# Optimization experiments

Measured on AMD Instinct MI355X. Metric: run time of the kernel, lower is better.

The kernel has to match this reference:

```python
import jax, jax.numpy as jnp
import numpy as np

B = 131072
UNITS = 256
INPUT_DIM = 256


def setup_inputs() -> dict:
    key = jax.random.key(0)
    ks = jax.random.split(key, 8)
    x = jax.random.normal(ks[0], (B, INPUT_DIM), dtype=jnp.float32)
    h_prev = jax.random.normal(ks[1], (B, UNITS), dtype=jnp.float32)
    c_prev = jax.random.normal(ks[2], (B, UNITS), dtype=jnp.float32)
    # glorot-like scale for W: fan_in = INPUT_DIM + UNITS, fan_out = 4*UNITS
    scale = jnp.sqrt(2.0 / (INPUT_DIM + UNITS + 4 * UNITS)).astype(jnp.float32)
    W = jax.random.normal(ks[3], (INPUT_DIM + UNITS, 4 * UNITS), dtype=jnp.float32) * scale
    # bias: zeros except forget gate initialized to 1.0
    b = jnp.concatenate([
        jnp.zeros(UNITS, jnp.float32),
        jnp.ones(UNITS, jnp.float32),
        jnp.zeros(UNITS, jnp.float32),
        jnp.zeros(UNITS, jnp.float32),
    ])
    peephole_i = jax.random.normal(ks[4], (UNITS,), dtype=jnp.float32) * 0.05
    peephole_f = jax.random.normal(ks[5], (UNITS,), dtype=jnp.float32) * 0.05
    peephole_o = jax.random.normal(ks[6], (UNITS,), dtype=jnp.float32) * 0.05
    return {
        "x": x, "h_prev": h_prev, "c_prev": c_prev,
        "W": W, "b": b,
        "peephole_i": peephole_i, "peephole_f": peephole_f, "peephole_o": peephole_o,
    }


def reference(x, h_prev, c_prev, W, b, peephole_i, peephole_f, peephole_o):
    combined = jnp.concatenate([x, h_prev], axis=-1)          # [B, INPUT_DIM+UNITS]
    z = combined @ W + b                                      # [B, 4*UNITS]
    i, f, c_hat, o = jnp.split(z, 4, axis=1)                  # each [B, UNITS]
    i = jax.nn.sigmoid(i + peephole_i * c_prev)
    f = jax.nn.sigmoid(f + peephole_f * c_prev)
    o = jax.nn.sigmoid(o + peephole_o * c_prev)
    c_hat = jnp.tanh(c_hat)
    c = f * c_prev + i * c_hat
    h = o * jnp.tanh(c)
    return (h, h, c)  # matches (output, [h, c]) of the Keras cell
```

## Files before the change

kernel.cpp:

```cpp
#include <hip/hip_runtime.h>
#include <cstdint>

#define NROWS   131072
#define NUNITS  256
#define KTOT    512
#define BM      128
#define THREADS 512

typedef float f32x4  __attribute__((ext_vector_type(4)));
typedef short bf16x8 __attribute__((ext_vector_type(8)));

__device__ __forceinline__ short f2bf(float x) {
    unsigned u = __float_as_uint(x);
    u += 0x7FFFu + ((u >> 16) & 1u);
    return (short)(u >> 16);
}

__global__ void convert_W_kernel(const float* __restrict__ W, short* __restrict__ Wws) {
    int i = blockIdx.x * 256 + threadIdx.x;
    int k = i >> 10;
    int c = i & 1023;
    Wws[((size_t)(k >> 5) << 15) + ((size_t)c << 5) + (k & 31)] = f2bf(W[i]);
}

__global__ void __launch_bounds__(THREADS, 4)
lstm_main_kernel(const float* __restrict__ x, const float* __restrict__ h_prev,
                 const float* __restrict__ c_prev, const float* __restrict__ bias,
                 const float* __restrict__ pi, const float* __restrict__ pf,
                 const float* __restrict__ po, const short* __restrict__ Wws,
                 float* __restrict__ out) {
    __shared__ short Ab[2][4096];
    __shared__ short Bb[3][8192];

    const int bid = blockIdx.x;
    const int swz = (bid & 7) * 512 + (bid >> 3);
    const int ut  = swz & 3;
    const int rt  = swz >> 2;
    const int row0 = rt * BM;

    const int t    = threadIdx.x;
    const int lane = t & 63;
    const int w    = t >> 6;
    const int lr   = lane & 15;
    const int hi   = lane >> 4;
    const int rh   = w >> 2;
    const int q    = w & 3;

    const int arow = t >> 2, ag = t & 3;
    const int avoff = ((row0 + arow) * 256 + ag * 8) * 4;
    const int awr   = arow * 32 + ((ag ^ ((arow >> 1) & 3)) * 8);

    const int u0  = (t >> 2) & 63;
    const int bg0 = t >> 8;
    const int bsw = ((t & 3) ^ ((t >> 3) & 3)) * 8;
    const int bvoff0 = (((bg0    ) * 256 + ut * 64 + u0) * 32 + bsw) * 2;
    const int bvoff1 = (((bg0 + 2) * 256 + ut * 64 + u0) * 32 + bsw) * 2;

    const int sw   = (hi ^ ((lr >> 1) & 3)) * 8;
    const int aoff = (rh * 64 + lr) * 32 + sw;
    const int boff = (q * 16 + lr) * 32 + sw;

    f32x4 acc[4][4];
    #pragma unroll
    for (int m = 0; m < 4; ++m)
        #pragma unroll
        for (int g = 0; g < 4; ++g)
            acc[m][g] = (f32x4){0.f, 0.f, 0.f, 0.f};

    f32x4 sreg[2];
    auto glbA = [&](int p) {
        const char* base = (const char*)(p < 8 ? x : h_prev) + ((p & 7) << 7);
        sreg[0] = *(const f32x4*)(base + avoff);
        sreg[1] = *(const f32x4*)(base + avoff + 16);
    };
    auto writeA = [&](int buf) {
        unsigned u0_, u1_, u2_, u3_;
        asm("v_cvt_pk_bf16_f32 %0, %1, %2" : "=v"(u0_) : "v"(sreg[0][0]), "v"(sreg[0][1]));
        asm("v_cvt_pk_bf16_f32 %0, %1, %2" : "=v"(u1_) : "v"(sreg[0][2]), "v"(sreg[0][3]));
        asm("v_cvt_pk_bf16_f32 %0, %1, %2" : "=v"(u2_) : "v"(sreg[1][0]), "v"(sreg[1][1]));
        asm("v_cvt_pk_bf16_f32 %0, %1, %2" : "=v"(u3_) : "v"(sreg[1][2]), "v"(sreg[1][3]));
        int4 v = make_int4((int)u0_, (int)u1_, (int)u2_, (int)u3_);
        *(int4*)&Ab[buf][awr] = v;
    };
    auto dmaB = [&](int p, int buf) {
        const char* wb = (const char*)Wws + ((size_t)p << 16);
        short* dst = &Bb[buf][0];
        __builtin_amdgcn_global_load_lds(
            (const __attribute__((address_space(1))) uint32_t*)(const void*)(wb + bvoff0),
            (__attribute__((address_space(3))) uint32_t*)(void*)(dst + t * 8), 16, 0, 0);
        __builtin_amdgcn_global_load_lds(
            (const __attribute__((address_space(1))) uint32_t*)(const void*)(wb + bvoff1),
            (__attribute__((address_space(3))) uint32_t*)(void*)(dst + 4096 + t * 8), 16, 0, 0);
    };
    auto compute = [&](int bufA, int bufB) {
        const short* A = &Ab[bufA][0];
        const short* B = &Bb[bufB][0];
        bf16x8 af[4], bfr[4];
        #pragma unroll
        for (int m = 0; m < 4; ++m)
            af[m] = *(const bf16x8*)&A[aoff + m * 512];
        #pragma unroll
        for (int g = 0; g < 4; ++g)
            bfr[g] = *(const bf16x8*)&B[boff + g * 2048];
        __builtin_amdgcn_s_setprio(1);
        #pragma unroll
        for (int g = 0; g < 4; ++g)
            #pragma unroll
            for (int m = 0; m < 4; ++m)
                acc[m][g] = __builtin_amdgcn_mfma_f32_16x16x32_bf16(af[m], bfr[g], acc[m][g], 0, 0, 0);
        __builtin_amdgcn_s_setprio(0);
    };

    glbA(0);
    dmaB(0, 0);
    dmaB(1, 1);
    writeA(0);
    asm volatile("s_waitcnt vmcnt(2) lgkmcnt(0)" ::: "memory");
    __builtin_amdgcn_s_barrier();

    #pragma unroll 2
    for (int p = 0; p < 16; ++p) {
        const int ca = p & 1, na = ca ^ 1;
        if (p < 15) glbA(p + 1);
        if (p < 14) dmaB(p + 2, (p + 2) % 3);
        compute(ca, p % 3);
        if (p < 15) {
            writeA(na);
            if (p < 14) { asm volatile("s_waitcnt vmcnt(2) lgkmcnt(0)" ::: "memory"); }
            else        { asm volatile("s_waitcnt vmcnt(0) lgkmcnt(0)" ::: "memory"); }
            __builtin_amdgcn_s_barrier();
        }
    }

    const size_t HS = (size_t)NROWS * NUNITS;
    const int u = ut * 64 + q * 16 + lr;
    const float bi = bias[u],       bfg = bias[256 + u];
    const float bc = bias[512 + u], bo  = bias[768 + u];
    const float ppi = pi[u], ppf = pf[u], ppo = po[u];
    #pragma unroll
    for (int m = 0; m < 4; ++m) {
        #pragma unroll
        for (int r = 0; r < 4; ++r) {
            const int row = row0 + rh * 64 + m * 16 + hi * 4 + r;
            const size_t o = (size_t)row * NUNITS + u;
            const float cp = c_prev[o];
            float zi = acc[m][0][r] + bi  + ppi * cp;
            float zf = acc[m][1][r] + bfg + ppf * cp;
            float zc = acc[m][2][r] + bc;
            float zo = acc[m][3][r] + bo  + ppo * cp;
            float ig = 1.f / (1.f + __expf(-zi));
            float fg = 1.f / (1.f + __expf(-zf));
            float og = 1.f / (1.f + __expf(-zo));
            zc = fminf(fmaxf(zc, -30.f), 30.f);
            float e2 = __expf(2.f * zc);
            float chat = (e2 - 1.f) / (e2 + 1.f);
            float c  = fg * cp + ig * chat;
            float ccl = fminf(fmaxf(c, -30.f), 30.f);
            float e3 = __expf(2.f * ccl);
            float th = (e3 - 1.f) / (e3 + 1.f);
            float h  = og * th;
            out[o]          = h;
            out[HS + o]     = h;
            out[2 * HS + o] = c;
        }
    }
}

extern "C" void kernel_launch(void* const* d_in, const int* in_sizes, int n_in,
                              void* d_out, int out_size, void* d_ws, size_t ws_size,
                              hipStream_t stream) {
    const float* x  = (const float*)d_in[0];
    const float* h  = (const float*)d_in[1];
    const float* c  = (const float*)d_in[2];
    const float* W  = (const float*)d_in[3];
    const float* b  = (const float*)d_in[4];
    const float* pi = (const float*)d_in[5];
    const float* pf = (const float*)d_in[6];
    const float* po = (const float*)d_in[7];
    float* out = (float*)d_out;

    short* Wws = (short*)d_ws;

    hipLaunchKernelGGL(convert_W_kernel, dim3(2048), dim3(256), 0, stream, W, Wws);
    hipLaunchKernelGGL(lstm_main_kernel, dim3(NROWS / BM * 4), dim3(THREADS), 0, stream,
                       x, h, c, b, pi, pf, po, Wws, out);
}
```

Measured before the change: 307.7 us.

## Double-buffer W tiles and prefetch activation registers two stages ahead

Replaces the triple-buffered LDS ring for W tiles with a double buffer. Activation global loads are now issued two k-steps ahead into a pair of register slots, and the next stage's A and B tiles are written before the current compute instead of after it. Dropping the third B buffer cuts shared memory per block, which may let more blocks share a CU. The trade-off is a shorter B prefetch distance and higher register pressure from the extra staging registers and the fully unrolled loop.

Result: faster. 301.7 us (median of 3 runs) (-2.0%).

```diff
diff --git a/kernel.cpp b/kernel.cpp
--- a/kernel.cpp
+++ b/kernel.cpp
@@ -30,7 +30,7 @@
                  const float* __restrict__ po, const short* __restrict__ Wws,
                  float* __restrict__ out) {
     __shared__ short Ab[2][4096];
-    __shared__ short Bb[3][8192];
+    __shared__ short Bb[2][8192];
 
     const int bid = blockIdx.x;
     const int swz = (bid & 7) * 512 + (bid >> 3);
@@ -67,24 +67,25 @@
         for (int g = 0; g < 4; ++g)
             acc[m][g] = (f32x4){0.f, 0.f, 0.f, 0.f};
 
-    f32x4 sreg[2];
+    f32x4 sreg[2][2];
     auto glbA = [&](int p) {
         const char* base = (const char*)(p < 8 ? x : h_prev) + ((p & 7) << 7);
-        sreg[0] = *(const f32x4*)(base + avoff);
-        sreg[1] = *(const f32x4*)(base + avoff + 16);
+        sreg[p & 1][0] = *(const f32x4*)(base + avoff);
+        sreg[p & 1][1] = *(const f32x4*)(base + avoff + 16);
     };
-    auto writeA = [&](int buf) {
+    auto writeA = [&](int p) {
+        const f32x4* s = sreg[p & 1];
         unsigned u0_, u1_, u2_, u3_;
-        asm("v_cvt_pk_bf16_f32 %0, %1, %2" : "=v"(u0_) : "v"(sreg[0][0]), "v"(sreg[0][1]));
-        asm("v_cvt_pk_bf16_f32 %0, %1, %2" : "=v"(u1_) : "v"(sreg[0][2]), "v"(sreg[0][3]));
-        asm("v_cvt_pk_bf16_f32 %0, %1, %2" : "=v"(u2_) : "v"(sreg[1][0]), "v"(sreg[1][1]));
-        asm("v_cvt_pk_bf16_f32 %0, %1, %2" : "=v"(u3_) : "v"(sreg[1][2]), "v"(sreg[1][3]));
+        asm("v_cvt_pk_bf16_f32 %0, %1, %2" : "=v"(u0_) : "v"(s[0][0]), "v"(s[0][1]));
+        asm("v_cvt_pk_bf16_f32 %0, %1, %2" : "=v"(u1_) : "v"(s[0][2]), "v"(s[0][3]));
+        asm("v_cvt_pk_bf16_f32 %0, %1, %2" : "=v"(u2_) : "v"(s[1][0]), "v"(s[1][1]));
+        asm("v_cvt_pk_bf16_f32 %0, %1, %2" : "=v"(u3_) : "v"(s[1][2]), "v"(s[1][3]));
         int4 v = make_int4((int)u0_, (int)u1_, (int)u2_, (int)u3_);
-        *(int4*)&Ab[buf][awr] = v;
+        *(int4*)&Ab[p & 1][awr] = v;
     };
-    auto dmaB = [&](int p, int buf) {
+    auto dmaB = [&](int p) {
         const char* wb = (const char*)Wws + ((size_t)p << 16);
-        short* dst = &Bb[buf][0];
+        short* dst = &Bb[p & 1][0];
         __builtin_amdgcn_global_load_lds(
             (const __attribute__((address_space(1))) uint32_t*)(const void*)(wb + bvoff0),
             (__attribute__((address_space(3))) uint32_t*)(void*)(dst + t * 8), 16, 0, 0);
@@ -92,9 +93,9 @@
             (const __attribute__((address_space(1))) uint32_t*)(const void*)(wb + bvoff1),
             (__attribute__((address_space(3))) uint32_t*)(void*)(dst + 4096 + t * 8), 16, 0, 0);
     };
-    auto compute = [&](int bufA, int bufB) {
-        const short* A = &Ab[bufA][0];
-        const short* B = &Bb[bufB][0];
+    auto compute = [&](int p) {
+        const short* A = &Ab[p & 1][0];
+        const short* B = &Bb[p & 1][0];
         bf16x8 af[4], bfr[4];
         #pragma unroll
         for (int m = 0; m < 4; ++m)
@@ -112,22 +113,23 @@
     };
 
     glbA(0);
-    dmaB(0, 0);
-    dmaB(1, 1);
+    dmaB(0);
+    glbA(1);
     writeA(0);
     asm volatile("s_waitcnt vmcnt(2) lgkmcnt(0)" ::: "memory");
     __builtin_amdgcn_s_barrier();
 
-    #pragma unroll 2
+    #pragma unroll
     for (int p = 0; p < 16; ++p) {
-        const int ca = p & 1, na = ca ^ 1;
-        if (p < 15) glbA(p + 1);
-        if (p < 14) dmaB(p + 2, (p + 2) % 3);
-        compute(ca, p % 3);
-        if (p < 15) {
-            writeA(na);
-            if (p < 14) { asm volatile("s_waitcnt vmcnt(2) lgkmcnt(0)" ::: "memory"); }
-            else        { asm volatile("s_waitcnt vmcnt(0) lgkmcnt(0)" ::: "memory"); }
+        if (p <= 14) dmaB(p + 1);
+        if (p <= 13) glbA(p + 2);
+        if (p <= 14) writeA(p + 1);
+        compute(p);
+        if (p <= 13) {
+            asm volatile("s_waitcnt vmcnt(2) lgkmcnt(0)" ::: "memory");
+            __builtin_amdgcn_s_barrier();
+        } else if (p == 14) {
+            asm volatile("s_waitcnt vmcnt(0) lgkmcnt(0)" ::: "memory");
             __builtin_amdgcn_s_barrier();
         }
     }
```
